# Kernel tuning notes

Hardware: AMD Instinct MI355X
Metric: run time of the kernel (lower is better)

The kernel has to match this reference:

```python
import jax, jax.numpy as jnp
import numpy as np

TEMPERATURE = 8.0  # sqrt(head_dim=64)


def setup_inputs() -> dict:
    key = jax.random.key(0)
    ks = jax.random.split(key, 6)
    B, H, S, D = 8, 8, 1024, 64
    shp = (B, H, S, D)
    names = ["q_r", "q_i", "k_r", "k_i", "v_r", "v_i"]
    return {n: jax.random.normal(k, shp, dtype=jnp.float32) for n, k in zip(names, ks)}


def _mag_minmax_norm(attn):
    """cvnn.MagMinMaxNorm(dim=-1): min-max normalize the magnitude along the
    last axis while preserving phase: x * (|x| - min) / ((max - min) * |x|)."""
    mag = jnp.abs(attn)                              # [B,H,Sq,Sk] real
    mn = jnp.min(mag, axis=-1, keepdims=True)
    mx = jnp.max(mag, axis=-1, keepdims=True)
    return attn * ((mag - mn) / ((mx - mn) * mag))


def reference(q_r, q_i, k_r, k_i, v_r, v_i):
    q = jax.lax.complex(q_r, q_i)
    k = jax.lax.complex(k_r, k_i)
    v = jax.lax.complex(v_r, v_i)
    # complex QK^T with temperature scaling
    attn = jnp.einsum("bhqd,bhkd->bhqk", q / TEMPERATURE, k)
    attn = _mag_minmax_norm(attn)
    # dropout is identity at inference (eval mode)
    out = jnp.einsum("bhqk,bhkd->bhqd", attn, v)
    # return real/imag stacked: [2, B, H, S, D]
    return jnp.stack([out.real, out.imag])
```

## Files before the change

### kernel.cpp

```cpp
#include <hip/hip_runtime.h>
#include <math.h>

typedef unsigned short ushort_t;
typedef __attribute__((ext_vector_type(8))) short short8;
typedef __attribute__((ext_vector_type(4))) float f32x4;
typedef __attribute__((ext_vector_type(4))) int int4v;

constexpr int S = 1024, D = 64, BH = 64;
constexpr int HALF = BH * S * D;
constexpr int KROW = 72;
constexpr int VROW = 72;
constexpr int TILE_USH = 2 * 32 * KROW + 64 * VROW;
constexpr int TILE_B = TILE_USH * 2;
constexpr size_t WS_NEED = (size_t)BH * 32 * TILE_B;

#define MFMA16(a, b, c) __builtin_amdgcn_mfma_f32_16x16x32_bf16(a, b, c, 0, 0, 0)

#if defined(__has_builtin)
#if __has_builtin(__builtin_amdgcn_cvt_pk_bf16_f32)
#define HAS_CVT_PK_BF16 1
typedef __attribute__((ext_vector_type(2))) __bf16 bf16x2_t;
__device__ __forceinline__ unsigned cvtpk(float a, float b) {
  bf16x2_t v = __builtin_amdgcn_cvt_pk_bf16_f32(a, b);
  unsigned u;
  __builtin_memcpy(&u, &v, 4);
  return u;
}
#endif
#endif
#ifndef HAS_CVT_PK_BF16
#define HAS_CVT_PK_BF16 0
__device__ __forceinline__ unsigned cvtpk(float a, float b) {
  __bf16 la = (__bf16)a, lb = (__bf16)b;
  unsigned short lo, hi;
  __builtin_memcpy(&lo, &la, 2);
  __builtin_memcpy(&hi, &lb, 2);
  return (unsigned)lo | ((unsigned)hi << 16);
}
#endif

__device__ __forceinline__ int4v pack8(float4 a, float4 b) {
  int4v r;
  r.x = (int)cvtpk(a.x, a.y);
  r.y = (int)cvtpk(a.z, a.w);
  r.z = (int)cvtpk(b.x, b.y);
  r.w = (int)cvtpk(b.z, b.w);
  return r;
}

__device__ __forceinline__ int4v twist4(int4v u) {
  int4v w;
  w.x = (int)((((unsigned)u.x >> 16) | ((unsigned)u.x << 16)) ^ 0x8000u);
  w.y = (int)((((unsigned)u.y >> 16) | ((unsigned)u.y << 16)) ^ 0x8000u);
  w.z = (int)((((unsigned)u.z >> 16) | ((unsigned)u.z << 16)) ^ 0x8000u);
  w.w = (int)((((unsigned)u.w >> 16) | ((unsigned)u.w << 16)) ^ 0x8000u);
  return w;
}

__global__ __launch_bounds__(256)
void prepass_kernel(const float* __restrict__ kr, const float* __restrict__ ki,
                    const float* __restrict__ vr, const float* __restrict__ vi,
                    ushort_t* __restrict__ ws) {
  __shared__ float svr[32 * 65], svi[32 * 65];
  const int t = threadIdx.x;
  const int tile = blockIdx.x;
  const size_t gbase = (size_t)tile * (32 * D);
  ushort_t* wst = ws + (size_t)tile * TILE_USH;
  const int k = t >> 3, d0 = (t & 7) * 8;
  const int dT = t >> 2, k0 = (t & 3) * 8;

  {
    float4 a = *(const float4*)(kr + gbase + k * D + d0);
    float4 b = *(const float4*)(kr + gbase + k * D + d0 + 4);
    *(int4v*)(wst + k * KROW + d0) = pack8(a, b);
  }
  {
    float4 a = *(const float4*)(ki + gbase + k * D + d0);
    float4 b = *(const float4*)(ki + gbase + k * D + d0 + 4);
    *(int4v*)(wst + 2304 + k * KROW + d0) = pack8(a, b);
  }
  {
    float4 a = *(const float4*)(vr + gbase + k * D + d0);
    float4 b = *(const float4*)(vr + gbase + k * D + d0 + 4);
    *(float4*)&svr[k * 65 + d0] = a;
    *(float4*)&svr[k * 65 + d0 + 4] = b;
    float4 c = *(const float4*)(vi + gbase + k * D + d0);
    float4 d = *(const float4*)(vi + gbase + k * D + d0 + 4);
    *(float4*)&svi[k * 65 + d0] = c;
    *(float4*)&svi[k * 65 + d0 + 4] = d;
  }
  __syncthreads();
  {
    unsigned dws[8];
#pragma unroll
    for (int j = 0; j < 8; ++j) {
      int s = k0 + j;
      dws[j] = cvtpk(svr[s * 65 + dT], -svi[s * 65 + dT]);
    }
    ushort_t* dst = wst + 4608 + dT * VROW + 2 * k0;
    *(int4v*)dst = *(int4v*)&dws[0];
    *(int4v*)(dst + 8) = *(int4v*)&dws[4];
  }
}

__global__ __launch_bounds__(256, 2)
void cvattn_mfma(const float* __restrict__ gq_r, const float* __restrict__ gq_i,
                 const ushort_t* __restrict__ ws, float* __restrict__ gout) {
  __shared__ __attribute__((aligned(16))) char smem[64512];
  ushort_t* sB = (ushort_t*)smem;
  const int t = threadIdx.x;
  const int lane = t & 63, wave = t >> 6;
  const int m = lane & 15, quad = lane >> 4;

  const int id = blockIdx.x;
  const int bh = (id & 7) * 8 + ((id >> 3) & 7);
  const int qt = id >> 6;
  const size_t base = (size_t)bh * (S * D);

  unsigned* pwu = (unsigned*)(smem + 27648) + wave * 2304;

  short8 fQr[2][2], fQi[2][2];
#pragma unroll
  for (int h = 0; h < 2; ++h) {
    const int row = qt * 128 + h * 64 + wave * 16 + m;
#pragma unroll
    for (int dc = 0; dc < 2; ++dc) {
      const int d = dc * 32 + quad * 8;
      const float* pr = gq_r + base + (size_t)row * D + d;
      const float* pi = gq_i + base + (size_t)row * D + d;
      int4v vr_ = pack8(*(const float4*)pr, *(const float4*)(pr + 4));
      int4v vi_ = pack8(*(const float4*)pi, *(const float4*)(pi + 4));
      __builtin_memcpy(&fQr[h][dc], &vr_, 16);
      __builtin_memcpy(&fQi[h][dc], &vi_, 16);
    }
  }

  f32x4 aAr[2][4] = {}, aAi[2][4] = {}, aUr[2][4] = {}, aUi[2][4] = {};
  float mn4[2][4], mx4[2][4];
#pragma unroll
  for (int h = 0; h < 2; ++h)
#pragma unroll
    for (int r = 0; r < 4; ++r) { mn4[h][r] = 1e30f; mx4[h][r] = 0.f; }

  const ushort_t* wsrc = ws + (size_t)bh * 32 * TILE_USH;

  int4v pre[5];
#pragma unroll
  for (int i = 0; i < 5; ++i) {
    int idx = i * 256 + t;
    if (idx < TILE_B / 16) pre[i] = *(const int4v*)(wsrc + idx * 8);
  }

  for (int kb = 0; kb < 32; ++kb) {
    __syncthreads();
#pragma unroll
    for (int i = 0; i < 5; ++i) {
      int idx = i * 256 + t;
      if (idx < TILE_B / 16) {
        *(int4v*)(smem + idx * 16) = pre[i];
        if (idx >= 576) *(int4v*)(smem + 18432 + (idx - 576) * 16) = twist4(pre[i]);
      }
    }
    if (kb + 1 < 32) {
      const ushort_t* g = wsrc + (size_t)(kb + 1) * TILE_USH;
#pragma unroll
      for (int i = 0; i < 5; ++i) {
        int idx = i * 256 + t;
        if (idx < TILE_B / 16) pre[i] = *(const int4v*)(g + idx * 8);
      }
    }
    __syncthreads();

#pragma unroll
    for (int ks = 0; ks < 2; ++ks) {
      const int krow = ks * 16 + m;
      short8 fKr0 = *(const short8*)&sB[krow * KROW + quad * 8];
      short8 fKr1 = *(const short8*)&sB[krow * KROW + 32 + quad * 8];
      short8 fKi0 = *(const short8*)&sB[2304 + krow * KROW + quad * 8];
      short8 fKi1 = *(const short8*)&sB[2304 + krow * KROW + 32 + quad * 8];
      short8 fKn0 = fKi0 ^ (short)0x8000;
      short8 fKn1 = fKi1 ^ (short)0x8000;
#pragma unroll
      for (int h = 0; h < 2; ++h) {
        f32x4 cSr = {}, cSi = {};
        cSr = MFMA16(fQr[h][0], fKr0, cSr);
        cSr = MFMA16(fQr[h][1], fKr1, cSr);
        cSr = MFMA16(fQi[h][0], fKn0, cSr);
        cSr = MFMA16(fQi[h][1], fKn1, cSr);
        cSi = MFMA16(fQr[h][0], fKi0, cSi);
        cSi = MFMA16(fQr[h][1], fKi1, cSi);
        cSi = MFMA16(fQi[h][0], fKr0, cSi);
        cSi = MFMA16(fQi[h][1], fKr1, cSi);
#pragma unroll
        for (int r = 0; r < 4; ++r) {
          float sr = cSr[r], si = cSi[r];
          float t2 = sr * sr + si * si;
          float rq = __builtin_amdgcn_rsqf(t2);
          mn4[h][r] = fminf(mn4[h][r], t2);
          mx4[h][r] = fmaxf(mx4[h][r], t2);
          const int dwo = h * 1152 + (quad * 4 + r) * 36 + ks * 16 + m;
          pwu[dwo] = cvtpk(sr, si);
          pwu[576 + dwo] = cvtpk(sr * rq, si * rq);
        }
      }
    }

    short8 fP0[2], fP1[2], fU0[2], fU1[2];
#pragma unroll
    for (int h = 0; h < 2; ++h) {
      const int bo = h * 1152 + m * 36 + quad * 4;
      fP0[h] = *(const short8*)&pwu[bo];
      fP1[h] = *(const short8*)&pwu[bo + 16];
      fU0[h] = *(const short8*)&pwu[576 + bo];
      fU1[h] = *(const short8*)&pwu[576 + bo + 16];
    }
#pragma unroll
    for (int dt = 0; dt < 4; ++dt) {
      const unsigned* vrow = (const unsigned*)sB + 2304 + (dt * 16 + m) * 36 + quad * 4;
      const unsigned* virow = vrow + 2304;
      short8 vre0 = *(const short8*)vrow;
      short8 vre1 = *(const short8*)(vrow + 16);
      short8 vim0 = *(const short8*)virow;
      short8 vim1 = *(const short8*)(virow + 16);
#pragma unroll
      for (int h = 0; h < 2; ++h) {
        aAr[h][dt] = MFMA16(fP0[h], vre0, aAr[h][dt]);
        aAr[h][dt] = MFMA16(fP1[h], vre1, aAr[h][dt]);
        aAi[h][dt] = MFMA16(fP0[h], vim0, aAi[h][dt]);
        aAi[h][dt] = MFMA16(fP1[h], vim1, aAi[h][dt]);
        aUr[h][dt] = MFMA16(fU0[h], vre0, aUr[h][dt]);
        aUr[h][dt] = MFMA16(fU1[h], vre1, aUr[h][dt]);
        aUi[h][dt] = MFMA16(fU0[h], vim0, aUi[h][dt]);
        aUi[h][dt] = MFMA16(fU1[h], vim1, aUi[h][dt]);
      }
    }
  }

#pragma unroll
  for (int h = 0; h < 2; ++h) {
    float inv[4];
#pragma unroll
    for (int r = 0; r < 4; ++r) {
#pragma unroll
      for (int mask = 1; mask < 16; mask <<= 1) {
        mn4[h][r] = fminf(mn4[h][r], __shfl_xor(mn4[h][r], mask, 64));
        mx4[h][r] = fmaxf(mx4[h][r], __shfl_xor(mx4[h][r], mask, 64));
      }
      mn4[h][r] = sqrtf(mn4[h][r]);
      mx4[h][r] = sqrtf(mx4[h][r]);
      inv[r] = 1.0f / (mx4[h][r] - mn4[h][r]);
    }
    const int qbase = qt * 128 + h * 64 + wave * 16 + quad * 4;
#pragma unroll
    for (int dt = 0; dt < 4; ++dt) {
      const int d = dt * 16 + m;
#pragma unroll
      for (int r = 0; r < 4; ++r) {
        size_t o = base + (size_t)(qbase + r) * D + d;
        gout[o] = (aAr[h][dt][r] - mn4[h][r] * aUr[h][dt][r]) * inv[r];
        gout[HALF + o] = (aAi[h][dt][r] - mn4[h][r] * aUi[h][dt][r]) * inv[r];
      }
    }
  }
}

constexpr int QT = 32, KT = 32;
constexpr int DP = D + 4;
constexpr int KP = KT + 1;

#define CDOT4(SR, SI, AR, AI, BR, BI)                              \
  SR += AR.x*BR.x + AR.y*BR.y + AR.z*BR.z + AR.w*BR.w              \
      - AI.x*BI.x - AI.y*BI.y - AI.z*BI.z - AI.w*BI.w;             \
  SI += AR.x*BI.x + AR.y*BI.y + AR.z*BI.z + AR.w*BI.w              \
      + AI.x*BR.x + AI.y*BR.y + AI.z*BR.z + AI.w*BR.w;

__global__ __launch_bounds__(256, 2)
void cvattn_fallback(const float* __restrict__ gq_r, const float* __restrict__ gq_i,
                     const float* __restrict__ gk_r, const float* __restrict__ gk_i,
                     const float* __restrict__ gv_r, const float* __restrict__ gv_i,
                     float* __restrict__ gout) {
  __shared__ float qs_r[QT][DP], qs_i[QT][DP];
  __shared__ float ks_r[KT][DP], ks_i[KT][DP];
  __shared__ float vs_r[KT][DP], vs_i[KT][DP];
  __shared__ float sc_r[QT][KP], sc_i[QT][KP], sc_m[QT][KP];
  const int t = threadIdx.x;
  const int qt2 = blockIdx.x, bh = blockIdx.y;
  const size_t base = (size_t)bh * (S * D);
  {
    const float* qr_p = gq_r + base + (size_t)qt2 * QT * D;
    const float* qi_p = gq_i + base + (size_t)qt2 * QT * D;
#pragma unroll
    for (int i = 0; i < 2; ++i) {
      int e = (t + i * 256) * 4;
      int row = e >> 6, col = e & 63;
      *(float4*)&qs_r[row][col] = *(const float4*)(qr_p + e);
      *(float4*)&qs_i[row][col] = *(const float4*)(qi_p + e);
    }
  }
  const int q0 = (t >> 4) * 2, k0 = (t & 15) * 2;
  const int rB = t >> 3, dc = (t & 7) * 8;
  float Ar[8] = {}, Ai[8] = {}, Ur[8] = {}, Ui[8] = {};
  float mn = 3.4e38f, mx = 0.0f;
  for (int kb = 0; kb < S / KT; ++kb) {
    __syncthreads();
    {
      const float* kr_p = gk_r + base + (size_t)kb * KT * D;
      const float* ki_p = gk_i + base + (size_t)kb * KT * D;
      const float* vr_p = gv_r + base + (size_t)kb * KT * D;
      const float* vi_p = gv_i + base + (size_t)kb * KT * D;
#pragma unroll
      for (int i = 0; i < 2; ++i) {
        int e = (t + i * 256) * 4;
        int row = e >> 6, col = e & 63;
        *(float4*)&ks_r[row][col] = *(const float4*)(kr_p + e);
        *(float4*)&ks_i[row][col] = *(const float4*)(ki_p + e);
        *(float4*)&vs_r[row][col] = *(const float4*)(vr_p + e);
        *(float4*)&vs_i[row][col] = *(const float4*)(vi_p + e);
      }
    }
    __syncthreads();
    {
      float s00r=0.f,s00i=0.f,s01r=0.f,s01i=0.f;
      float s10r=0.f,s10i=0.f,s11r=0.f,s11i=0.f;
#pragma unroll
      for (int d = 0; d < D; d += 4) {
        float4 a0r = *(const float4*)&qs_r[q0  ][d];
        float4 a0i = *(const float4*)&qs_i[q0  ][d];
        float4 a1r = *(const float4*)&qs_r[q0+1][d];
        float4 a1i = *(const float4*)&qs_i[q0+1][d];
        float4 b0r = *(const float4*)&ks_r[k0  ][d];
        float4 b0i = *(const float4*)&ks_i[k0  ][d];
        float4 b1r = *(const float4*)&ks_r[k0+1][d];
        float4 b1i = *(const float4*)&ks_i[k0+1][d];
        CDOT4(s00r, s00i, a0r, a0i, b0r, b0i);
        CDOT4(s01r, s01i, a0r, a0i, b1r, b1i);
        CDOT4(s10r, s10i, a1r, a1i, b0r, b0i);
        CDOT4(s11r, s11i, a1r, a1i, b1r, b1i);
      }
      s00r *= 0.125f; s00i *= 0.125f; s01r *= 0.125f; s01i *= 0.125f;
      s10r *= 0.125f; s10i *= 0.125f; s11r *= 0.125f; s11i *= 0.125f;
      sc_r[q0  ][k0  ] = s00r; sc_i[q0  ][k0  ] = s00i;
      sc_m[q0  ][k0  ] = sqrtf(s00r*s00r + s00i*s00i);
      sc_r[q0  ][k0+1] = s01r; sc_i[q0  ][k0+1] = s01i;
      sc_m[q0  ][k0+1] = sqrtf(s01r*s01r + s01i*s01i);
      sc_r[q0+1][k0  ] = s10r; sc_i[q0+1][k0  ] = s10i;
      sc_m[q0+1][k0  ] = sqrtf(s10r*s10r + s10i*s10i);
      sc_r[q0+1][k0+1] = s11r; sc_i[q0+1][k0+1] = s11i;
      sc_m[q0+1][k0+1] = sqrtf(s11r*s11r + s11i*s11i);
    }
    __syncthreads();
#pragma unroll 8
    for (int k = 0; k < KT; ++k) {
      float sr = sc_r[rB][k], si = sc_i[rB][k], mg = sc_m[rB][k];
      mn = fminf(mn, mg); mx = fmaxf(mx, mg);
      float inv = 1.0f / mg;
      float ur = sr * inv, ui = si * inv;
      float vr[8], vi[8];
      *(float4*)&vr[0] = *(const float4*)&vs_r[k][dc];
      *(float4*)&vr[4] = *(const float4*)&vs_r[k][dc + 4];
      *(float4*)&vi[0] = *(const float4*)&vs_i[k][dc];
      *(float4*)&vi[4] = *(const float4*)&vs_i[k][dc + 4];
#pragma unroll
      for (int j = 0; j < 8; ++j) {
        Ar[j] += sr * vr[j] - si * vi[j];
        Ai[j] += sr * vi[j] + si * vr[j];
        Ur[j] += ur * vr[j] - ui * vi[j];
        Ui[j] += ur * vi[j] + ui * vr[j];
      }
    }
  }
  float invspan = 1.0f / (mx - mn);
  float outr[8], outi[8];
#pragma unroll
  for (int j = 0; j < 8; ++j) {
    outr[j] = (Ar[j] - mn * Ur[j]) * invspan;
    outi[j] = (Ai[j] - mn * Ui[j]) * invspan;
  }
  size_t o = base + (size_t)(qt2 * QT + rB) * D + dc;
  *(float4*)(gout + o)            = *(float4*)&outr[0];
  *(float4*)(gout + o + 4)        = *(float4*)&outr[4];
  *(float4*)(gout + HALF + o)     = *(float4*)&outi[0];
  *(float4*)(gout + HALF + o + 4) = *(float4*)&outi[4];
}

extern "C" void kernel_launch(void* const* d_in, const int* in_sizes, int n_in,
                              void* d_out, int out_size, void* d_ws, size_t ws_size,
                              hipStream_t stream) {
  if (ws_size >= WS_NEED) {
    prepass_kernel<<<dim3(BH * 32), 256, 0, stream>>>(
        (const float*)d_in[2], (const float*)d_in[3],
        (const float*)d_in[4], (const float*)d_in[5], (ushort_t*)d_ws);
    cvattn_mfma<<<dim3(S / 128 * BH), 256, 0, stream>>>(
        (const float*)d_in[0], (const float*)d_in[1],
        (const ushort_t*)d_ws, (float*)d_out);
  } else {
    cvattn_fallback<<<dim3(S / QT, BH), 256, 0, stream>>>(
        (const float*)d_in[0], (const float*)d_in[1],
        (const float*)d_in[2], (const float*)d_in[3],
        (const float*)d_in[4], (const float*)d_in[5], (float*)d_out);
  }
}
```

Baseline: 248.4 us.

## Keep score fragments in registers via transposed QK MFMA and double-buffer K/V tiles

Swaps the operand order of the QK^T MFMAs so each lane's score output already matches the A-operand layout needed by the PV MFMAs. This removes the per-wave LDS round trip for the P/U fragments and shrinks shared memory. K/V tiles are now double-buffered in LDS with one barrier per iteration instead of two. The twisted imaginary V copy is built in registers rather than stored to LDS, and the min/max reduction now runs across quads instead of within rows. The cost is more register pressure and extra ALU work per PV step.

```diff
diff --git a/kernel.cpp b/kernel.cpp
--- a/kernel.cpp
+++ b/kernel.cpp
@@ -48,13 +48,17 @@
   return r;
 }
 
-__device__ __forceinline__ int4v twist4(int4v u) {
+__device__ __forceinline__ short8 twist(short8 v) {
+  int4v u;
+  __builtin_memcpy(&u, &v, 16);
   int4v w;
   w.x = (int)((((unsigned)u.x >> 16) | ((unsigned)u.x << 16)) ^ 0x8000u);
   w.y = (int)((((unsigned)u.y >> 16) | ((unsigned)u.y << 16)) ^ 0x8000u);
   w.z = (int)((((unsigned)u.z >> 16) | ((unsigned)u.z << 16)) ^ 0x8000u);
   w.w = (int)((((unsigned)u.w >> 16) | ((unsigned)u.w << 16)) ^ 0x8000u);
-  return w;
+  short8 r;
+  __builtin_memcpy(&r, &w, 16);
+  return r;
 }
 
 __global__ __launch_bounds__(256)
@@ -106,7 +110,7 @@
 __global__ __launch_bounds__(256, 2)
 void cvattn_mfma(const float* __restrict__ gq_r, const float* __restrict__ gq_i,
                  const ushort_t* __restrict__ ws, float* __restrict__ gout) {
-  __shared__ __attribute__((aligned(16))) char smem[64512];
+  __shared__ __attribute__((aligned(16))) char smem[2 * 18432];
   ushort_t* sB = (ushort_t*)smem;
   const int t = threadIdx.x;
   const int lane = t & 63, wave = t >> 6;
@@ -117,9 +121,7 @@
   const int qt = id >> 6;
   const size_t base = (size_t)bh * (S * D);
 
-  unsigned* pwu = (unsigned*)(smem + 27648) + wave * 2304;
-
-  short8 fQr[2][2], fQi[2][2];
+  short8 fQr[2][2], fQi[2][2], fQn[2][2];
 #pragma unroll
   for (int h = 0; h < 2; ++h) {
     const int row = qt * 128 + h * 64 + wave * 16 + m;
@@ -132,15 +134,12 @@
       int4v vi_ = pack8(*(const float4*)pi, *(const float4*)(pi + 4));
       __builtin_memcpy(&fQr[h][dc], &vr_, 16);
       __builtin_memcpy(&fQi[h][dc], &vi_, 16);
+      fQn[h][dc] = fQi[h][dc] ^ (short)0x8000;
     }
   }
 
   f32x4 aAr[2][4] = {}, aAi[2][4] = {}, aUr[2][4] = {}, aUi[2][4] = {};
-  float mn4[2][4], mx4[2][4];
-#pragma unroll
-  for (int h = 0; h < 2; ++h)
-#pragma unroll
-    for (int r = 0; r < 4; ++r) { mn4[h][r] = 1e30f; mx4[h][r] = 0.f; }
+  float mn2[2] = {1e30f, 1e30f}, mx2[2] = {0.f, 0.f};
 
   const ushort_t* wsrc = ws + (size_t)bh * 32 * TILE_USH;
 
@@ -150,78 +149,82 @@
     int idx = i * 256 + t;
     if (idx < TILE_B / 16) pre[i] = *(const int4v*)(wsrc + idx * 8);
   }
+#pragma unroll
+  for (int i = 0; i < 5; ++i) {
+    int idx = i * 256 + t;
+    if (idx < TILE_B / 16) *(int4v*)(smem + idx * 16) = pre[i];
+  }
+#pragma unroll
+  for (int i = 0; i < 5; ++i) {
+    int idx = i * 256 + t;
+    if (idx < TILE_B / 16) pre[i] = *(const int4v*)(wsrc + TILE_USH + idx * 8);
+  }
+  __syncthreads();
 
   for (int kb = 0; kb < 32; ++kb) {
-    __syncthreads();
-#pragma unroll
-    for (int i = 0; i < 5; ++i) {
-      int idx = i * 256 + t;
-      if (idx < TILE_B / 16) {
-        *(int4v*)(smem + idx * 16) = pre[i];
-        if (idx >= 576) *(int4v*)(smem + 18432 + (idx - 576) * 16) = twist4(pre[i]);
-      }
-    }
-    if (kb + 1 < 32) {
-      const ushort_t* g = wsrc + (size_t)(kb + 1) * TILE_USH;
-#pragma unroll
-      for (int i = 0; i < 5; ++i) {
-        int idx = i * 256 + t;
-        if (idx < TILE_B / 16) pre[i] = *(const int4v*)(g + idx * 8);
-      }
-    }
-    __syncthreads();
-
+    const int cur = kb & 1;
+    const int cbu = cur * 9216;
+    const int cbd = cur * 4608;
+
+    short8 fP0[2], fP1[2], fU0[2], fU1[2];
 #pragma unroll
     for (int ks = 0; ks < 2; ++ks) {
       const int krow = ks * 16 + m;
-      short8 fKr0 = *(const short8*)&sB[krow * KROW + quad * 8];
-      short8 fKr1 = *(const short8*)&sB[krow * KROW + 32 + quad * 8];
-      short8 fKi0 = *(const short8*)&sB[2304 + krow * KROW + quad * 8];
-      short8 fKi1 = *(const short8*)&sB[2304 + krow * KROW + 32 + quad * 8];
-      short8 fKn0 = fKi0 ^ (short)0x8000;
-      short8 fKn1 = fKi1 ^ (short)0x8000;
+      short8 fKr0 = *(const short8*)&sB[cbu + krow * KROW + quad * 8];
+      short8 fKr1 = *(const short8*)&sB[cbu + krow * KROW + 32 + quad * 8];
+      short8 fKi0 = *(const short8*)&sB[cbu + 2304 + krow * KROW + quad * 8];
+      short8 fKi1 = *(const short8*)&sB[cbu + 2304 + krow * KROW + 32 + quad * 8];
 #pragma unroll
       for (int h = 0; h < 2; ++h) {
         f32x4 cSr = {}, cSi = {};
-        cSr = MFMA16(fQr[h][0], fKr0, cSr);
-        cSr = MFMA16(fQr[h][1], fKr1, cSr);
-        cSr = MFMA16(fQi[h][0], fKn0, cSr);
-        cSr = MFMA16(fQi[h][1], fKn1, cSr);
-        cSi = MFMA16(fQr[h][0], fKi0, cSi);
-        cSi = MFMA16(fQr[h][1], fKi1, cSi);
-        cSi = MFMA16(fQi[h][0], fKr0, cSi);
-        cSi = MFMA16(fQi[h][1], fKr1, cSi);
+        cSr = MFMA16(fKr0, fQr[h][0], cSr);
+        cSr = MFMA16(fKr1, fQr[h][1], cSr);
+        cSr = MFMA16(fKi0, fQn[h][0], cSr);
+        cSr = MFMA16(fKi1, fQn[h][1], cSr);
+        cSi = MFMA16(fKi0, fQr[h][0], cSi);
+        cSi = MFMA16(fKi1, fQr[h][1], cSi);
+        cSi = MFMA16(fKr0, fQi[h][0], cSi);
+        cSi = MFMA16(fKr1, fQi[h][1], cSi);
+        unsigned pd[4], ud[4];
 #pragma unroll
         for (int r = 0; r < 4; ++r) {
           float sr = cSr[r], si = cSi[r];
           float t2 = sr * sr + si * si;
           float rq = __builtin_amdgcn_rsqf(t2);
-          mn4[h][r] = fminf(mn4[h][r], t2);
-          mx4[h][r] = fmaxf(mx4[h][r], t2);
-          const int dwo = h * 1152 + (quad * 4 + r) * 36 + ks * 16 + m;
-          pwu[dwo] = cvtpk(sr, si);
-          pwu[576 + dwo] = cvtpk(sr * rq, si * rq);
+          mn2[h] = fminf(mn2[h], t2);
+          mx2[h] = fmaxf(mx2[h], t2);
+          pd[r] = cvtpk(sr, si);
+          ud[r] = cvtpk(sr * rq, si * rq);
         }
-      }
-    }
-
-    short8 fP0[2], fP1[2], fU0[2], fU1[2];
-#pragma unroll
-    for (int h = 0; h < 2; ++h) {
-      const int bo = h * 1152 + m * 36 + quad * 4;
-      fP0[h] = *(const short8*)&pwu[bo];
-      fP1[h] = *(const short8*)&pwu[bo + 16];
-      fU0[h] = *(const short8*)&pwu[576 + bo];
-      fU1[h] = *(const short8*)&pwu[576 + bo + 16];
-    }
+        if (ks == 0) { __builtin_memcpy(&fP0[h], pd, 16); __builtin_memcpy(&fU0[h], ud, 16); }
+        else         { __builtin_memcpy(&fP1[h], pd, 16); __builtin_memcpy(&fU1[h], ud, 16); }
+      }
+    }
+
+    if (kb + 1 < 32) {
+      char* dst = smem + (cur ^ 1) * 18432;
+#pragma unroll
+      for (int i = 0; i < 5; ++i) {
+        int idx = i * 256 + t;
+        if (idx < TILE_B / 16) *(int4v*)(dst + idx * 16) = pre[i];
+      }
+    }
+    if (kb + 2 < 32) {
+      const ushort_t* g = wsrc + (size_t)(kb + 2) * TILE_USH;
+#pragma unroll
+      for (int i = 0; i < 5; ++i) {
+        int idx = i * 256 + t;
+        if (idx < TILE_B / 16) pre[i] = *(const int4v*)(g + idx * 8);
+      }
+    }
+
 #pragma unroll
     for (int dt = 0; dt < 4; ++dt) {
-      const unsigned* vrow = (const unsigned*)sB + 2304 + (dt * 16 + m) * 36 + quad * 4;
-      const unsigned* virow = vrow + 2304;
+      const unsigned* vrow = (const unsigned*)sB + cbd + 2304 + (dt * 16 + m) * 36 + quad * 4;
       short8 vre0 = *(const short8*)vrow;
       short8 vre1 = *(const short8*)(vrow + 16);
-      short8 vim0 = *(const short8*)virow;
-      short8 vim1 = *(const short8*)(virow + 16);
+      short8 vim0 = twist(vre0);
+      short8 vim1 = twist(vre1);
 #pragma unroll
       for (int h = 0; h < 2; ++h) {
         aAr[h][dt] = MFMA16(fP0[h], vre0, aAr[h][dt]);
@@ -234,31 +237,30 @@
         aUi[h][dt] = MFMA16(fU1[h], vim1, aUi[h][dt]);
       }
     }
+    __syncthreads();
   }
 
 #pragma unroll
   for (int h = 0; h < 2; ++h) {
-    float inv[4];
+#pragma unroll
+    for (int mask = 16; mask < 64; mask <<= 1) {
+      mn2[h] = fminf(mn2[h], __shfl_xor(mn2[h], mask, 64));
+      mx2[h] = fmaxf(mx2[h], __shfl_xor(mx2[h], mask, 64));
+    }
+    const float mnv = sqrtf(mn2[h]);
+    const float invv = 1.0f / (sqrtf(mx2[h]) - mnv);
+    const int qbase = qt * 128 + h * 64 + wave * 16 + quad * 4;
 #pragma unroll
     for (int r = 0; r < 4; ++r) {
-#pragma unroll
-      for (int mask = 1; mask < 16; mask <<= 1) {
-        mn4[h][r] = fminf(mn4[h][r], __shfl_xor(mn4[h][r], mask, 64));
-        mx4[h][r] = fmaxf(mx4[h][r], __shfl_xor(mx4[h][r], mask, 64));
-      }
-      mn4[h][r] = sqrtf(mn4[h][r]);
-      mx4[h][r] = sqrtf(mx4[h][r]);
-      inv[r] = 1.0f / (mx4[h][r] - mn4[h][r]);
-    }
-    const int qbase = qt * 128 + h * 64 + wave * 16 + quad * 4;
-#pragma unroll
-    for (int dt = 0; dt < 4; ++dt) {
-      const int d = dt * 16 + m;
-#pragma unroll
-      for (int r = 0; r < 4; ++r) {
+      const int src = quad * 4 + r;
+      const float mnr = __shfl(mnv, src, 64);
+      const float ivr = __shfl(invv, src, 64);
+#pragma unroll
+      for (int dt = 0; dt < 4; ++dt) {
+        const int d = dt * 16 + m;
         size_t o = base + (size_t)(qbase + r) * D + d;
-        gout[o] = (aAr[h][dt][r] - mn4[h][r] * aUr[h][dt][r]) * inv[r];
-        gout[HALF + o] = (aAi[h][dt][r] - mn4[h][r] * aUi[h][dt][r]) * inv[r];
+        gout[o] = (aAr[h][dt][r] - mnr * aUr[h][dt][r]) * ivr;
+        gout[HALF + o] = (aAi[h][dt][r] - mnr * aUi[h][dt][r]) * ivr;
       }
     }
   }
```

Result: slower. 254.2 us (+2.3%).
